# Kernel tuning notes

Hardware: AMD Instinct MI355X
Metric: run time of the kernel (lower is better)

## Reference

```python
import jax, jax.numpy as jnp
import numpy as np
import math

B, S, D, H = 2, 2048, 1024, 16
DK = D // H


def setup_inputs() -> dict:
    key = jax.random.key(0)
    ks = jax.random.split(key, 12)
    s = 0.02
    return {
        "query": jax.random.normal(ks[0], (B, S, D), jnp.float32),
        "key": jax.random.normal(ks[1], (B, S, D), jnp.float32),
        "value": jax.random.normal(ks[2], (B, S, D), jnp.float32),
        "mask": jnp.zeros((1, 1, S, S), jnp.float32),
        "Wq": jax.random.normal(ks[3], (D, D), jnp.float32) * s,
        "bq": jnp.zeros((D,), jnp.float32),
        "Wk": jax.random.normal(ks[4], (D, D), jnp.float32) * s,
        "bk": jnp.zeros((D,), jnp.float32),
        "Wv": jax.random.normal(ks[5], (D, D), jnp.float32) * s,
        "bv": jnp.zeros((D,), jnp.float32),
        "Wpost": jax.random.normal(ks[6], (D, D), jnp.float32) * s,
        "bpost": jnp.zeros((D,), jnp.float32),
        "per_dim_scale": jnp.zeros((DK,), jnp.float32),
    }


def reference(query, key, value, mask, Wq, bq, Wk, bk, Wv, bv, Wpost, bpost, per_dim_scale):
    # Linear projections (torch Linear: x @ W.T + b), split heads -> [B, H, S, DK]
    def proj(x, W, b):
        return (x @ W.T + b).reshape(B, S, H, DK).transpose(0, 2, 1, 3)

    q = proj(query, Wq, bq)
    k = proj(key, Wk, bk)
    v = proj(value, Wv, bv)

    # PerDimScale: scale = (1/ln2) / sqrt(d_k) * softplus(per_dim_scale)
    r_softplus_0 = 1.442695041
    scale = (r_softplus_0 / math.sqrt(DK)) * jax.nn.softplus(per_dim_scale)
    q = q * scale  # broadcast over last dim

    # Full attention matrix [B, H, S, S] + additive mask + softmax (dropout p=0)
    attn = jnp.einsum('bhqd,bhkd->bhqk', q, k) + mask
    attn = jax.nn.softmax(attn, axis=-1)

    out = jnp.einsum('bhqk,bhkd->bhqd', attn, v)
    out = out.transpose(0, 2, 1, 3).reshape(B, S, D)
    return out @ Wpost.T + bpost
```

## Files before the change

kernel.cpp:

```cpp
#include <hip/hip_runtime.h>
#include <math.h>

typedef __bf16 bf16;
typedef __bf16 bf16x8 __attribute__((ext_vector_type(8)));
typedef float f32x4 __attribute__((ext_vector_type(4)));

static constexpr int NB = 2, NS = 2048, ND = 1024, NH = 16, NDK = 64;
static constexpr float LOG2E = 1.442695041f;

__device__ __forceinline__ f32x4 mfma16(bf16x8 a, bf16x8 b, f32x4 c) {
  return __builtin_amdgcn_mfma_f32_16x16x32_bf16(a, b, c, 0, 0, 0);
}

__device__ __forceinline__ float exp2_fast(float x) {
  return __builtin_amdgcn_exp2f(x);
}

__device__ __forceinline__ void gload16(const void* g, void* l) {
  __builtin_amdgcn_global_load_lds(
      (const __attribute__((address_space(1))) void*)g,
      (__attribute__((address_space(3))) void*)l, 16, 0, 0);
}

__global__ void scale_kernel(const float* __restrict__ pds, float* __restrict__ scale) {
  int i = threadIdx.x;
  if (i < NDK) {
    float x = pds[i];
    float sp = fmaxf(x, 0.0f) + log1pf(expf(-fabsf(x)));
    scale[i] = (LOG2E * LOG2E / 8.0f) * sp;
  }
}

__global__ void maskflag_kernel(const float* __restrict__ mask, int* __restrict__ flag, int n4) {
  int idx = blockIdx.x * blockDim.x + threadIdx.x;
  int stride = gridDim.x * blockDim.x;
  unsigned acc = 0;
  for (int i = idx; i < n4; i += stride) {
    float4 v = ((const float4*)mask)[i];
    acc |= (__float_as_uint(v.x) << 1) | (__float_as_uint(v.y) << 1)
         | (__float_as_uint(v.z) << 1) | (__float_as_uint(v.w) << 1);
  }
  if (acc != 0) atomicOr(flag, 1);
}

__global__ __launch_bounds__(256) void cvt_bf16(
    const float* __restrict__ s0, const float* __restrict__ s1,
    const float* __restrict__ s2, const float* __restrict__ s3,
    bf16* __restrict__ d0, bf16* __restrict__ d1,
    bf16* __restrict__ d2, bf16* __restrict__ d3, int n8) {
  const float* s = blockIdx.y == 0 ? s0 : blockIdx.y == 1 ? s1 : blockIdx.y == 2 ? s2 : s3;
  bf16* d = blockIdx.y == 0 ? d0 : blockIdx.y == 1 ? d1 : blockIdx.y == 2 ? d2 : d3;
  for (int i = blockIdx.x * 256 + threadIdx.x; i < n8; i += gridDim.x * 256) {
    const float4* f = (const float4*)s + 2 * (size_t)i;
    float4 a = f[0], b = f[1];
    bf16x8 o;
    o[0] = (bf16)a.x; o[1] = (bf16)a.y; o[2] = (bf16)a.z; o[3] = (bf16)a.w;
    o[4] = (bf16)b.x; o[5] = (bf16)b.y; o[6] = (bf16)b.z; o[7] = (bf16)b.w;
    *((bf16x8*)d + i) = o;
  }
}

__global__ __launch_bounds__(256) void qkv_mm(
    const bf16* __restrict__ Xq, const bf16* __restrict__ Xk, const bf16* __restrict__ Xv,
    const bf16* __restrict__ Wqb, const bf16* __restrict__ Wkb, const bf16* __restrict__ Wvb,
    const float* __restrict__ bq, const float* __restrict__ bk, const float* __restrict__ bv,
    const float* __restrict__ scale2,
    bf16* __restrict__ Qs, bf16* __restrict__ Ks, bf16* __restrict__ Vt, int mode0) {
  __shared__ __align__(16) bf16 la[128 * 64];
  __shared__ __align__(16) bf16 lb[128 * 64];
  const int which = mode0 + blockIdx.y;
  const bf16* A  = which == 0 ? Xq  : which == 1 ? Xk  : Wvb;
  const bf16* Bm = which == 0 ? Wqb : which == 1 ? Wkb : Xv;
  const int t = threadIdx.x, lane = t & 63, wave = t >> 6;
  const int wm = wave >> 1, wn = wave & 1;
  int bm, bn;
  if (which == 2) { bm = blockIdx.x & 7; bn = blockIdx.x >> 3; }
  else            { bm = blockIdx.x >> 3; bn = blockIdx.x & 7; }
  const int g = lane >> 4, l15 = lane & 15;
  const int sr = wave * 8 + (lane >> 3);
  const int sc = ((lane & 7) ^ (lane >> 3)) * 8;
  const bf16* Abase = A  + (size_t)(bm * 128) * ND;
  const bf16* Bbase = Bm + (size_t)(bn * 128) * ND;

  f32x4 acc[4][4] = {};

  for (int kt = 0; kt < ND; kt += 64) {
    for (int c = 0; c < 4; ++c) {
      gload16(Abase + (size_t)(c * 32 + sr) * ND + kt + sc, la + c * 2048 + wave * 512);
      gload16(Bbase + (size_t)(c * 32 + sr) * ND + kt + sc, lb + c * 2048 + wave * 512);
    }
    __syncthreads();
    __builtin_amdgcn_s_setprio(1);
    for (int kk = 0; kk < 2; ++kk) {
      bf16x8 af[4], bfv[4];
      for (int m = 0; m < 4; ++m) {
        const int rr = wm * 64 + m * 16 + l15;
        af[m] = *(const bf16x8*)&la[rr * 64 + (((g + 4 * kk) ^ (rr & 7)) << 3)];
      }
      for (int n = 0; n < 4; ++n) {
        const int rr = wn * 64 + n * 16 + l15;
        bfv[n] = *(const bf16x8*)&lb[rr * 64 + (((g + 4 * kk) ^ (rr & 7)) << 3)];
      }
      for (int m = 0; m < 4; ++m)
        for (int n = 0; n < 4; ++n)
          acc[m][n] = mfma16(af[m], bfv[n], acc[m][n]);
    }
    __builtin_amdgcn_s_setprio(0);
    __syncthreads();
  }

  const int lr4 = g * 4;
  if (which != 2) {
    const float* bias = which ? bk : bq;
    bf16* outp = which ? Ks : Qs;
    for (int m = 0; m < 4; ++m) {
      const int grow0 = bm * 128 + wm * 64 + m * 16 + lr4;
      for (int n = 0; n < 4; ++n) {
        const int gcol = bn * 128 + wn * 64 + n * 16 + l15;
        const int h = gcol >> 6, dk = gcol & 63;
        const float bia = bias[gcol];
        const float sc2 = which ? 1.0f : scale2[dk];
        for (int r = 0; r < 4; ++r) {
          const int grow = grow0 + r;
          float v = acc[m][n][r] + bia;
          if (which == 0) v *= sc2;
          const int bb = grow >> 11, s = grow & (NS - 1);
          outp[(((size_t)(bb * NH + h)) * NS + s) * NDK + dk] = (bf16)v;
        }
      }
    }
  } else {
    for (int m = 0; m < 4; ++m) {
      const int d0 = bm * 128 + wm * 64 + m * 16 + lr4;
      for (int n = 0; n < 4; ++n) {
        const int gcol = bn * 128 + wn * 64 + n * 16 + l15;
        const int bb = gcol >> 11, s = gcol & (NS - 1);
        for (int r = 0; r < 4; ++r) {
          const int d = d0 + r;
          const float v = acc[m][n][r] + bv[d];
          const int h = d >> 6, dk = d & 63;
          Vt[(((size_t)(bb * NH + h)) * NDK + dk) * NS + s] = (bf16)v;
        }
      }
    }
  }
}

__global__ __launch_bounds__(256) void post_mm2(
    const bf16* __restrict__ A, const bf16* __restrict__ Bm,
    const float* __restrict__ bias, float* __restrict__ out) {
  __shared__ __align__(16) bf16 la[2][64 * 64];
  __shared__ __align__(16) bf16 lb[2][128 * 64];
  const int t = threadIdx.x, lane = t & 63, wave = t >> 6;
  const int bm = blockIdx.x >> 3, bn = blockIdx.x & 7;
  const int g = lane >> 4, l15 = lane & 15;
  const int sr = wave * 8 + (lane >> 3);
  const int sc = ((lane & 7) ^ (lane >> 3)) * 8;
  const bf16* Abase = A  + (size_t)(bm * 64) * ND;
  const bf16* Bbase = Bm + (size_t)(bn * 128) * ND;

  f32x4 acc[4][2] = {};

  auto stage = [&](int kt, int b) {
    for (int c = 0; c < 2; ++c)
      gload16(Abase + (size_t)(c * 32 + sr) * ND + kt + sc, la[b] + c * 2048 + wave * 512);
    for (int c = 0; c < 4; ++c)
      gload16(Bbase + (size_t)(c * 32 + sr) * ND + kt + sc, lb[b] + c * 2048 + wave * 512);
  };

  stage(0, 0);
  asm volatile("s_waitcnt vmcnt(0)" ::: "memory");
  __builtin_amdgcn_s_barrier();

  for (int it = 0; it < 16; ++it) {
    const int cur = it & 1;
    if (it + 1 < 16) stage((it + 1) * 64, cur ^ 1);

    __builtin_amdgcn_s_setprio(1);
    for (int kk = 0; kk < 2; ++kk) {
      bf16x8 af[4], bfv[2];
      for (int m = 0; m < 4; ++m) {
        const int rr = m * 16 + l15;
        af[m] = *(const bf16x8*)&la[cur][rr * 64 + (((g + 4 * kk) ^ (rr & 7)) << 3)];
      }
      for (int n = 0; n < 2; ++n) {
        const int rr = wave * 32 + n * 16 + l15;
        bfv[n] = *(const bf16x8*)&lb[cur][rr * 64 + (((g + 4 * kk) ^ (rr & 7)) << 3)];
      }
      for (int m = 0; m < 4; ++m)
        for (int n = 0; n < 2; ++n)
          acc[m][n] = mfma16(af[m], bfv[n], acc[m][n]);
    }
    __builtin_amdgcn_s_setprio(0);

    asm volatile("s_waitcnt vmcnt(0)" ::: "memory");
    __builtin_amdgcn_s_barrier();
  }

  for (int m = 0; m < 4; ++m) {
    const int grow0 = bm * 64 + m * 16 + g * 4;
    for (int n = 0; n < 2; ++n) {
      const int gcol = bn * 128 + wave * 32 + n * 16 + l15;
      const float bia = bias[gcol];
      for (int r = 0; r < 4; ++r)
        out[(size_t)(grow0 + r) * ND + gcol] = acc[m][n][r] + bia;
    }
  }
}

__global__ __launch_bounds__(512) void attn5(
    const bf16* __restrict__ Qs, const bf16* __restrict__ Ks,
    const bf16* __restrict__ Vt, const float* __restrict__ mask,
    const int* __restrict__ flag, bf16* __restrict__ Obs) {
  __shared__ __align__(16) bf16 lk[2 * 64 * 64];
  __shared__ __align__(16) bf16 lv[2 * 64 * 64];
  __shared__ __align__(16) bf16 lp[8 * 16 * 64];

  const int t = threadIdx.x, lane = t & 63, wave = t >> 6;
  const int g = lane >> 4, l15 = lane & 15;
  const int bh = blockIdx.y;
  const int qbase = blockIdx.x * 128 + wave * 16;
  const bool use_mask = (*flag) != 0;

  const bf16* Qh = Qs + (size_t)bh * NS * NDK;
  const bf16* Kh = Ks + (size_t)bh * NS * NDK;
  const bf16* Vh = Vt + (size_t)bh * NDK * NS;

  bf16x8 qf[2];
#pragma unroll
  for (int kk = 0; kk < 2; ++kk)
    qf[kk] = *(const bf16x8*)&Qh[(size_t)(qbase + l15) * NDK + kk * 32 + g * 8];

  f32x4 o_acc[4] = {};
  float lsum[4] = {0.0f, 0.0f, 0.0f, 0.0f};

  unsigned kfo[2][4];
#pragma unroll
  for (int kk = 0; kk < 2; ++kk)
#pragma unroll
    for (int n = 0; n < 4; ++n)
      kfo[kk][n] = (unsigned)((n * 16 + l15) * 64 + (((g + 4 * kk) ^ (l15 & 7)) << 3));
  unsigned pwo[4][4];
#pragma unroll
  for (int n = 0; n < 4; ++n)
#pragma unroll
    for (int r = 0; r < 4; ++r) {
      const int q = g * 4 + r;
      pwo[n][r] = (unsigned)(wave * 1024 + q * 64 + ((n * 16 + l15) ^ ((q & 7) << 3)));
    }
  unsigned pro[2];
#pragma unroll
  for (int kk = 0; kk < 2; ++kk)
    pro[kk] = (unsigned)(wave * 1024 + l15 * 64 + ((kk * 32 + g * 8) ^ ((l15 & 7) << 3)));

  const int srow = wave * 8 + (lane >> 3);
  const int sc = ((lane & 7) ^ (lane >> 3)) * 8;

  auto stage = [&](int kv, int b) {
    gload16(Kh + (size_t)(kv + srow) * NDK + sc, lk + b * 4096 + wave * 512);
    gload16(Vh + (size_t)srow * NS + kv + sc, lv + b * 4096 + wave * 512);
  };

  auto body = [&](int kv, int cur) {
    if (kv + 64 < NS) stage(kv + 64, cur ^ 1);

    f32x4 sacc[4] = {};
    __builtin_amdgcn_s_setprio(1);
#pragma unroll
    for (int kk = 0; kk < 2; ++kk)
#pragma unroll
      for (int n = 0; n < 4; ++n)
        sacc[n] = mfma16(qf[kk], *(const bf16x8*)&lk[cur * 4096 + kfo[kk][n]], sacc[n]);
    __builtin_amdgcn_s_setprio(0);

    if (use_mask) {
#pragma unroll
      for (int n = 0; n < 4; ++n)
#pragma unroll
        for (int r = 0; r < 4; ++r)
          sacc[n][r] += LOG2E * mask[(size_t)(qbase + g * 4 + r) * NS + kv + n * 16 + l15];
    }

#pragma unroll
    for (int n = 0; n < 4; ++n)
#pragma unroll
      for (int r = 0; r < 4; ++r) {
        const float e = exp2_fast(sacc[n][r]);
        lsum[r] += e;
        lp[pwo[n][r]] = (bf16)e;
      }

#pragma unroll
    for (int kk = 0; kk < 2; ++kk) {
      const bf16x8 pf = *(const bf16x8*)&lp[pro[kk]];
      __builtin_amdgcn_s_setprio(1);
#pragma unroll
      for (int n = 0; n < 4; ++n)
        o_acc[n] = mfma16(pf, *(const bf16x8*)&lv[cur * 4096 + kfo[kk][n]], o_acc[n]);
      __builtin_amdgcn_s_setprio(0);
    }

    asm volatile("s_waitcnt vmcnt(0)" ::: "memory");
    __builtin_amdgcn_s_barrier();
  };

  stage(0, 0);
  asm volatile("s_waitcnt vmcnt(0)" ::: "memory");
  __builtin_amdgcn_s_barrier();

  for (int kv = 0; kv < NS; kv += 128) {
    body(kv, 0);
    body(kv + 64, 1);
  }

  const int bidx = bh >> 4, h = bh & 15;
#pragma unroll
  for (int r = 0; r < 4; ++r) {
    float rs = lsum[r];
    rs += __shfl_xor(rs, 1, 64);
    rs += __shfl_xor(rs, 2, 64);
    rs += __shfl_xor(rs, 4, 64);
    rs += __shfl_xor(rs, 8, 64);
    const float rinv = 1.0f / rs;
    const int qrow = qbase + g * 4 + r;
#pragma unroll
    for (int n = 0; n < 4; ++n)
      Obs[((size_t)(bidx * NS + qrow)) * ND + h * 64 + n * 16 + l15] = (bf16)(o_acc[n][r] * rinv);
  }
}

extern "C" void kernel_launch(void* const* d_in, const int* in_sizes, int n_in,
                              void* d_out, int out_size, void* d_ws, size_t ws_size,
                              hipStream_t stream) {
  (void)in_sizes; (void)n_in; (void)out_size;
  const float* query = (const float*)d_in[0];
  const float* key   = (const float*)d_in[1];
  const float* value = (const float*)d_in[2];
  const float* mask  = (const float*)d_in[3];
  const float* Wq    = (const float*)d_in[4];
  const float* bq    = (const float*)d_in[5];
  const float* Wk    = (const float*)d_in[6];
  const float* bk    = (const float*)d_in[7];
  const float* Wv    = (const float*)d_in[8];
  const float* bv    = (const float*)d_in[9];
  const float* Wpost = (const float*)d_in[10];
  const float* bpost = (const float*)d_in[11];
  const float* pds   = (const float*)d_in[12];

  char* ws = (char*)d_ws;
  const size_t MB = 1u << 20;
  bf16* Xq  = (bf16*)(ws + 0 * MB);
  bf16* Xk  = (bf16*)(ws + 8 * MB);
  bf16* Xv  = (bf16*)(ws + 16 * MB);
  bf16* Wqb = (bf16*)(ws + 24 * MB);
  bf16* Wkb = (bf16*)(ws + 26 * MB);
  bf16* Wvb = (bf16*)(ws + 28 * MB);
  bf16* Wpb = (bf16*)(ws + 30 * MB);
  float* scale2 = (float*)(ws + 32 * MB);
  int* flag     = (int*)(ws + 32 * MB + 256);

  const bool fused = ws_size >= (size_t)50 * MB;
  bf16 *Qsp, *Ksp, *Vtp, *Obsp;
  if (fused) {
    Qsp = (bf16*)d_out;
    Ksp = (bf16*)((char*)d_out + 8 * MB);
    Vtp = (bf16*)(ws + 33 * MB);
    Obsp = (bf16*)(ws + 41 * MB);
  } else {
    Qsp = (bf16*)d_out;
    Ksp = Xq;
    Vtp = Xk;
    Obsp = Xv;
  }

  (void)hipMemsetAsync(flag, 0, sizeof(int), stream);
  scale_kernel<<<1, 64, 0, stream>>>(pds, scale2);
  maskflag_kernel<<<256, 256, 0, stream>>>(mask, flag, NS * NS / 4);

  cvt_bf16<<<dim3(512, 3), 256, 0, stream>>>(query, key, value, nullptr,
                                             Xq, Xk, Xv, nullptr, NB * NS * ND / 8);
  cvt_bf16<<<dim3(512, 4), 256, 0, stream>>>(Wq, Wk, Wv, Wpost,
                                             Wqb, Wkb, Wvb, Wpb, ND * ND / 8);

  if (fused) {
    qkv_mm<<<dim3(256, 3), 256, 0, stream>>>(Xq, Xk, Xv, Wqb, Wkb, Wvb,
                                             bq, bk, bv, scale2, Qsp, Ksp, Vtp, 0);
  } else {
    qkv_mm<<<dim3(256, 1), 256, 0, stream>>>(Xq, Xk, Xv, Wqb, Wkb, Wvb,
                                             bq, bk, bv, scale2, Qsp, Ksp, Vtp, 0);
    qkv_mm<<<dim3(256, 1), 256, 0, stream>>>(Xq, Xk, Xv, Wqb, Wkb, Wvb,
                                             bq, bk, bv, scale2, Qsp, Ksp, Vtp, 1);
    qkv_mm<<<dim3(256, 1), 256, 0, stream>>>(Xq, Xk, Xv, Wqb, Wkb, Wvb,
                                             bq, bk, bv, scale2, Qsp, Ksp, Vtp, 2);
  }

  attn5<<<dim3(16, 32), 512, 0, stream>>>(Qsp, Ksp, Vtp, mask, flag, Obsp);

  post_mm2<<<512, 256, 0, stream>>>(Obsp, Wpb, bpost, (float*)d_out);
}
```

Measured before the change: 136.1 us.

## Deepen attention K/V pipeline to four buffers and interleave QK/PV; merge prep launches

The attention kernel now uses four LDS buffers for K and V, loading two 64-key tiles per stage. It processes tile pairs so the second tile's QK^T MFMAs are issued before the first tile's PV, which lets exp work overlap with matrix work and halves the barriers. Separately, the scale and mask-flag kernels are merged into one launch, and the activation and weight bf16 conversions are merged into one launch. This costs double the LDS for K/V, which may lower occupancy, and raises register pressure from holding two score tiles at once.

```diff
diff --git a/kernel.cpp b/kernel.cpp
--- a/kernel.cpp
+++ b/kernel.cpp
@@ -22,18 +22,19 @@
       (__attribute__((address_space(3))) void*)l, 16, 0, 0);
 }
 
-__global__ void scale_kernel(const float* __restrict__ pds, float* __restrict__ scale) {
-  int i = threadIdx.x;
-  if (i < NDK) {
-    float x = pds[i];
-    float sp = fmaxf(x, 0.0f) + log1pf(expf(-fabsf(x)));
-    scale[i] = (LOG2E * LOG2E / 8.0f) * sp;
-  }
-}
-
-__global__ void maskflag_kernel(const float* __restrict__ mask, int* __restrict__ flag, int n4) {
+__global__ void prep_kernel(const float* __restrict__ pds, float* __restrict__ scale,
+                            const float* __restrict__ mask, int* __restrict__ flag, int n4) {
+  if (blockIdx.x == 256) {
+    int i = threadIdx.x;
+    if (i < NDK) {
+      float x = pds[i];
+      float sp = fmaxf(x, 0.0f) + log1pf(expf(-fabsf(x)));
+      scale[i] = (LOG2E * LOG2E / 8.0f) * sp;
+    }
+    return;
+  }
   int idx = blockIdx.x * blockDim.x + threadIdx.x;
-  int stride = gridDim.x * blockDim.x;
+  int stride = 256 * blockDim.x;
   unsigned acc = 0;
   for (int i = idx; i < n4; i += stride) {
     float4 v = ((const float4*)mask)[i];
@@ -44,12 +45,18 @@
 }
 
 __global__ __launch_bounds__(256) void cvt_bf16(
-    const float* __restrict__ s0, const float* __restrict__ s1,
-    const float* __restrict__ s2, const float* __restrict__ s3,
-    bf16* __restrict__ d0, bf16* __restrict__ d1,
-    bf16* __restrict__ d2, bf16* __restrict__ d3, int n8) {
-  const float* s = blockIdx.y == 0 ? s0 : blockIdx.y == 1 ? s1 : blockIdx.y == 2 ? s2 : s3;
-  bf16* d = blockIdx.y == 0 ? d0 : blockIdx.y == 1 ? d1 : blockIdx.y == 2 ? d2 : d3;
+    const float* __restrict__ s0, const float* __restrict__ s1, const float* __restrict__ s2,
+    const float* __restrict__ s3, const float* __restrict__ s4, const float* __restrict__ s5,
+    const float* __restrict__ s6,
+    bf16* __restrict__ d0, bf16* __restrict__ d1, bf16* __restrict__ d2,
+    bf16* __restrict__ d3, bf16* __restrict__ d4, bf16* __restrict__ d5,
+    bf16* __restrict__ d6, int n8x, int n8w) {
+  const int y = blockIdx.y;
+  const float* s = y == 0 ? s0 : y == 1 ? s1 : y == 2 ? s2 : y == 3 ? s3
+                 : y == 4 ? s4 : y == 5 ? s5 : s6;
+  bf16* d = y == 0 ? d0 : y == 1 ? d1 : y == 2 ? d2 : y == 3 ? d3
+          : y == 4 ? d4 : y == 5 ? d5 : d6;
+  const int n8 = y < 3 ? n8x : n8w;
   for (int i = blockIdx.x * 256 + threadIdx.x; i < n8; i += gridDim.x * 256) {
     const float4* f = (const float4*)s + 2 * (size_t)i;
     float4 a = f[0], b = f[1];
@@ -208,12 +215,12 @@
   }
 }
 
-__global__ __launch_bounds__(512) void attn5(
+__global__ __launch_bounds__(512) void attn6(
     const bf16* __restrict__ Qs, const bf16* __restrict__ Ks,
     const bf16* __restrict__ Vt, const float* __restrict__ mask,
     const int* __restrict__ flag, bf16* __restrict__ Obs) {
-  __shared__ __align__(16) bf16 lk[2 * 64 * 64];
-  __shared__ __align__(16) bf16 lv[2 * 64 * 64];
+  __shared__ __align__(16) bf16 lk[4 * 64 * 64];
+  __shared__ __align__(16) bf16 lv[4 * 64 * 64];
   __shared__ __align__(16) bf16 lp[8 * 16 * 64];
 
   const int t = threadIdx.x, lane = t & 63, wave = t >> 6;
@@ -261,35 +268,35 @@
     gload16(Vh + (size_t)srow * NS + kv + sc, lv + b * 4096 + wave * 512);
   };
 
-  auto body = [&](int kv, int cur) {
-    if (kv + 64 < NS) stage(kv + 64, cur ^ 1);
-
-    f32x4 sacc[4] = {};
+  auto qkt = [&](int kv, int cur, f32x4 (&s)[4]) {
     __builtin_amdgcn_s_setprio(1);
 #pragma unroll
     for (int kk = 0; kk < 2; ++kk)
 #pragma unroll
       for (int n = 0; n < 4; ++n)
-        sacc[n] = mfma16(qf[kk], *(const bf16x8*)&lk[cur * 4096 + kfo[kk][n]], sacc[n]);
+        s[n] = mfma16(qf[kk], *(const bf16x8*)&lk[cur * 4096 + kfo[kk][n]], s[n]);
     __builtin_amdgcn_s_setprio(0);
-
     if (use_mask) {
 #pragma unroll
       for (int n = 0; n < 4; ++n)
 #pragma unroll
         for (int r = 0; r < 4; ++r)
-          sacc[n][r] += LOG2E * mask[(size_t)(qbase + g * 4 + r) * NS + kv + n * 16 + l15];
-    }
-
+          s[n][r] += LOG2E * mask[(size_t)(qbase + g * 4 + r) * NS + kv + n * 16 + l15];
+    }
+  };
+
+  auto expw = [&](f32x4 (&s)[4]) {
 #pragma unroll
     for (int n = 0; n < 4; ++n)
 #pragma unroll
       for (int r = 0; r < 4; ++r) {
-        const float e = exp2_fast(sacc[n][r]);
+        const float e = exp2_fast(s[n][r]);
         lsum[r] += e;
         lp[pwo[n][r]] = (bf16)e;
       }
-
+  };
+
+  auto pv = [&](int cur) {
 #pragma unroll
     for (int kk = 0; kk < 2; ++kk) {
       const bf16x8 pf = *(const bf16x8*)&lp[pro[kk]];
@@ -299,18 +306,30 @@
         o_acc[n] = mfma16(pf, *(const bf16x8*)&lv[cur * 4096 + kfo[kk][n]], o_acc[n]);
       __builtin_amdgcn_s_setprio(0);
     }
-
+  };
+
+  auto pair = [&](int kv, int cA, int cB, int sA, int sB, bool doStage) {
+    if (doStage) { stage(kv + 128, sA); stage(kv + 192, sB); }
+    f32x4 sa[4] = {};
+    qkt(kv, cA, sa);
+    expw(sa);
+    f32x4 sb[4] = {};
+    qkt(kv + 64, cB, sb);
+    pv(cA);
+    expw(sb);
+    pv(cB);
     asm volatile("s_waitcnt vmcnt(0)" ::: "memory");
     __builtin_amdgcn_s_barrier();
   };
 
   stage(0, 0);
+  stage(64, 1);
   asm volatile("s_waitcnt vmcnt(0)" ::: "memory");
   __builtin_amdgcn_s_barrier();
 
-  for (int kv = 0; kv < NS; kv += 128) {
-    body(kv, 0);
-    body(kv + 64, 1);
+  for (int p = 0; p < 16; p += 2) {
+    pair(p * 128,       0, 1, 2, 3, true);
+    pair(p * 128 + 128, 2, 3, 0, 1, p != 14);
   }
 
   const int bidx = bh >> 4, h = bh & 15;
@@ -374,13 +393,11 @@
   }
 
   (void)hipMemsetAsync(flag, 0, sizeof(int), stream);
-  scale_kernel<<<1, 64, 0, stream>>>(pds, scale2);
-  maskflag_kernel<<<256, 256, 0, stream>>>(mask, flag, NS * NS / 4);
-
-  cvt_bf16<<<dim3(512, 3), 256, 0, stream>>>(query, key, value, nullptr,
-                                             Xq, Xk, Xv, nullptr, NB * NS * ND / 8);
-  cvt_bf16<<<dim3(512, 4), 256, 0, stream>>>(Wq, Wk, Wv, Wpost,
-                                             Wqb, Wkb, Wvb, Wpb, ND * ND / 8);
+  prep_kernel<<<257, 256, 0, stream>>>(pds, scale2, mask, flag, NS * NS / 4);
+
+  cvt_bf16<<<dim3(256, 7), 256, 0, stream>>>(query, key, value, Wq, Wk, Wv, Wpost,
+                                             Xq, Xk, Xv, Wqb, Wkb, Wvb, Wpb,
+                                             NB * NS * ND / 8, ND * ND / 8);
 
   if (fused) {
     qkv_mm<<<dim3(256, 3), 256, 0, stream>>>(Xq, Xk, Xv, Wqb, Wkb, Wvb,
@@ -394,7 +411,7 @@
                                              bq, bk, bv, scale2, Qsp, Ksp, Vtp, 2);
   }
 
-  attn5<<<dim3(16, 32), 512, 0, stream>>>(Qsp, Ksp, Vtp, mask, flag, Obsp);
+  attn6<<<dim3(16, 32), 512, 0, stream>>>(Qsp, Ksp, Vtp, mask, flag, Obsp);
 
   post_mm2<<<512, 256, 0, stream>>>(Obsp, Wpb, bpost, (float*)d_out);
 }
```

Measured after the change: 143.9 us. 5.7% more time.
